# Kernel optimization log

Measured on AMD Instinct MI355X. Metric: run time of the kernel, lower is better.

The kernel has to match this reference:

```python
import jax, jax.numpy as jnp
import numpy as np

B, N, DIM = 8, 4096, 128

def setup_inputs() -> dict:
    key = jax.random.key(0)
    ks = jax.random.split(key, 6)
    s = 1.0 / np.sqrt(DIM)
    return {
        "x": jax.random.normal(ks[0], (B, N, DIM), dtype=jnp.float32),
        "q_global": jax.random.normal(ks[1], (B, N, DIM), dtype=jnp.float32),
        "Wkv": jax.random.normal(ks[2], (DIM, 2 * DIM), dtype=jnp.float32) * s,
        "bkv": jax.random.normal(ks[3], (2 * DIM,), dtype=jnp.float32) * 0.02,
        "Wp": jax.random.normal(ks[4], (DIM, DIM), dtype=jnp.float32) * s,
        "bp": jax.random.normal(ks[5], (DIM,), dtype=jnp.float32) * 0.02,
    }

def reference(x, q_global, Wkv, bkv, Wp, bp):
    # x: [B, n, dim]; kv linear -> split into k, v (each [B, n, dim])
    kv = x @ Wkv + bkv
    k, v = jnp.split(kv, 2, axis=-1)
    dim = x.shape[-1]
    q = q_global * (1.0 / jnp.sqrt(jnp.asarray(dim, x.dtype)))
    # scores = k @ q^T : [B, n, m]; softmax over query axis m (as in source)
    scores = jnp.einsum("bnd,bmd->bnm", k, q)
    attn = jax.nn.softmax(scores, axis=-1)
    # attention @ v : contracts m against v's row index (m == n)
    out = jnp.einsum("bnm,bmd->bnd", attn, v)
    return out @ Wp + bp
```

## Files before the change

kernel.cpp:

```cpp
#include <hip/hip_runtime.h>

typedef __bf16 bf16x8 __attribute__((ext_vector_type(8)));
typedef float f32x4 __attribute__((ext_vector_type(4)));

struct alignas(16) US8 { unsigned short us[8]; };

static __device__ inline unsigned short f2bf(float f) {
  union { float f; unsigned u; } v; v.f = f;
  unsigned r = v.u + 0x7fffu + ((v.u >> 16) & 1u);
  return (unsigned short)(r >> 16);
}

#define NSEQ 4096
#define DIM 128
#define ROWS 32768
#define KH 2

#define EXPC (1.4426950408889634f * 0.08838834764831845f)

__global__ void prep_kernel(const float* __restrict__ Wkv, const float* __restrict__ Wp,
                            unsigned short* __restrict__ wkvT, unsigned short* __restrict__ wpT) {
  const int t = threadIdx.x;
  if (blockIdx.x == 0) {
    for (int d = 0; d < 128; ++d)
      wkvT[t * 128 + d] = f2bf(Wkv[d * 256 + t]);
  } else {
    const int col = t & 127, d0 = (t >> 7) * 64;
    for (int d = d0; d < d0 + 64; ++d)
      wpT[col * 128 + d] = f2bf(Wp[d * 128 + col]);
  }
}

__global__ __launch_bounds__(256, 2) void kv_kernel(
    const float* __restrict__ x, const unsigned short* __restrict__ wkvT,
    const float* __restrict__ bkv, const float* __restrict__ q,
    unsigned short* __restrict__ kout, unsigned short* __restrict__ vtout,
    unsigned short* __restrict__ qo) {
  const int tid = threadIdx.x;
  if (blockIdx.x >= 512) {
    int i = ((blockIdx.x - 512) * 256 + tid) * 8;
    const float4* p = reinterpret_cast<const float4*>(q + i);
    float4 a = p[0], b = p[1];
    US8 o;
    o.us[0]=f2bf(a.x*EXPC); o.us[1]=f2bf(a.y*EXPC); o.us[2]=f2bf(a.z*EXPC); o.us[3]=f2bf(a.w*EXPC);
    o.us[4]=f2bf(b.x*EXPC); o.us[5]=f2bf(b.y*EXPC); o.us[6]=f2bf(b.z*EXPC); o.us[7]=f2bf(b.w*EXPC);
    *reinterpret_cast<US8*>(qo + i) = o;
    return;
  }
  __shared__ __align__(16) unsigned short WT[128 * 136];
  const int wv = tid >> 6, lane = tid & 63, l16 = lane & 15, quad = lane >> 4;
  const int h = blockIdx.x & 1, rb = blockIdx.x >> 1;
  const int row0 = rb * 128;
  const unsigned short* wsrc = wkvT + h * 128 * 128;

  for (int p = 0; p < 8; ++p) {
    int c = p * 256 + tid;
    int col = c >> 4, c16 = c & 15;
    *reinterpret_cast<US8*>(&WT[col * 136 + c16 * 8]) =
        *reinterpret_cast<const US8*>(wsrc + col * 128 + c16 * 8);
  }
  __syncthreads();

  f32x4 acc[2][8];
  for (int rg = 0; rg < 2; ++rg)
    for (int g = 0; g < 8; ++g) acc[rg][g] = f32x4{0.f, 0.f, 0.f, 0.f};
  for (int rg = 0; rg < 2; ++rg) {
    const int arow = row0 + wv * 32 + rg * 16 + l16;
    for (int s = 0; s < 4; ++s) {
      const float4* xp = reinterpret_cast<const float4*>(x + (size_t)arow * DIM + s * 32 + quad * 8);
      float4 u0 = xp[0], u1 = xp[1];
      US8 af;
      af.us[0]=f2bf(u0.x); af.us[1]=f2bf(u0.y); af.us[2]=f2bf(u0.z); af.us[3]=f2bf(u0.w);
      af.us[4]=f2bf(u1.x); af.us[5]=f2bf(u1.y); af.us[6]=f2bf(u1.z); af.us[7]=f2bf(u1.w);
      bf16x8 a = __builtin_bit_cast(bf16x8, af);
      for (int g = 0; g < 8; ++g) {
        bf16x8 bfr = *reinterpret_cast<const bf16x8*>(&WT[(g * 16 + l16) * 136 + s * 32 + quad * 8]);
        acc[rg][g] = __builtin_amdgcn_mfma_f32_16x16x32_bf16(a, bfr, acc[rg][g], 0, 0, 0);
      }
    }
  }

  if (h == 0) {
    for (int rg = 0; rg < 2; ++rg)
      for (int g = 0; g < 8; ++g) {
        float bias = bkv[g * 16 + l16];
        for (int r = 0; r < 4; ++r) {
          int orow = row0 + wv * 32 + rg * 16 + quad * 4 + r;
          kout[(size_t)orow * DIM + g * 16 + l16] = f2bf(acc[rg][g][r] + bias);
        }
      }
  } else {
    __syncthreads();
    unsigned short* LDSt = WT;
    for (int rg = 0; rg < 2; ++rg)
      for (int g = 0; g < 8; ++g) {
        float bias = bkv[128 + g * 16 + l16];
        for (int r = 0; r < 4; ++r)
          LDSt[(g * 16 + l16) * 136 + wv * 32 + rg * 16 + quad * 4 + r] = f2bf(acc[rg][g][r] + bias);
      }
    __syncthreads();
    const int bb = row0 >> 12, n0 = row0 & (NSEQ - 1);
    unsigned short* vb = vtout + (size_t)bb * NSEQ * DIM;
    for (int p = 0; p < 8; ++p) {
      int c = p * 256 + tid;
      int d = c >> 4, c8 = c & 15;
      *reinterpret_cast<US8*>(vb + (size_t)d * NSEQ + n0 + c8 * 8) =
          *reinterpret_cast<const US8*>(&LDSt[d * 136 + c8 * 8]);
    }
  }
}

__global__ __launch_bounds__(256, 2) void attn_kernel(
    const unsigned short* __restrict__ kbuf, const unsigned short* __restrict__ qbuf,
    const unsigned short* __restrict__ vtbuf,
    float* __restrict__ opart, float* __restrict__ lpart) {
  __shared__ __align__(16) unsigned short SH[27136];
  const int tid = threadIdx.x;
  const int wv = tid >> 6, lane = tid & 63, l16 = lane & 15, quad = lane >> 4;
  const int b = blockIdx.x & 7;
  const int t = blockIdx.x >> 3;
  const int q0 = (t & 31) * 128;
  const int kh = t >> 5;
  const int key0 = kh * (NSEQ / KH);
  const unsigned short* kb = kbuf + (size_t)b * NSEQ * DIM;
  const unsigned short* qb = qbuf + (size_t)b * NSEQ * DIM;
  const unsigned short* vtb = vtbuf + (size_t)b * NSEQ * DIM;

  unsigned short* Ksh  = SH;
  unsigned short* VTsh = SH + 8704;
  unsigned short* pp   = SH + 17920 + wv * 2304;

  bf16x8 afrag[2][4];
  for (int rg = 0; rg < 2; ++rg) {
    const int arow = q0 + wv * 32 + rg * 16 + l16;
    for (int s = 0; s < 4; ++s)
      afrag[rg][s] = __builtin_bit_cast(bf16x8,
          *reinterpret_cast<const US8*>(kb + (size_t)arow * DIM + s * 32 + quad * 8));
  }

  f32x4 Oacc[2][8];
  for (int rg = 0; rg < 2; ++rg)
    for (int g = 0; g < 8; ++g) Oacc[rg][g] = f32x4{0.f, 0.f, 0.f, 0.f};
  float lsum[2][4];
  for (int rg = 0; rg < 2; ++rg)
    for (int r = 0; r < 4; ++r) lsum[rg][r] = 0.f;

  for (int it = 0; it < NSEQ / KH / 64; ++it) {
    const int m0 = key0 + it * 64;
    __syncthreads();
    for (int p = 0; p < 4; ++p) {
      int c = p * 256 + tid;
      int row = c >> 4, c16 = c & 15;
      *reinterpret_cast<US8*>(&Ksh[row * 136 + c16 * 8]) =
          *reinterpret_cast<const US8*>(qb + (size_t)(m0 + row) * DIM + c16 * 8);
    }
    for (int p = 0; p < 4; ++p) {
      int c = p * 256 + tid;
      int d = c >> 3, c8 = c & 7;
      *reinterpret_cast<US8*>(&VTsh[d * 72 + c8 * 8]) =
          *reinterpret_cast<const US8*>(vtb + (size_t)d * NSEQ + m0 + c8 * 8);
    }
    __syncthreads();

    f32x4 S[2][4];
    for (int rg = 0; rg < 2; ++rg)
      for (int g = 0; g < 4; ++g) S[rg][g] = f32x4{0.f, 0.f, 0.f, 0.f};
    for (int s = 0; s < 4; ++s)
      for (int g = 0; g < 4; ++g) {
        bf16x8 bfr = *reinterpret_cast<const bf16x8*>(&Ksh[(g * 16 + l16) * 136 + s * 32 + quad * 8]);
        S[0][g] = __builtin_amdgcn_mfma_f32_16x16x32_bf16(afrag[0][s], bfr, S[0][g], 0, 0, 0);
        S[1][g] = __builtin_amdgcn_mfma_f32_16x16x32_bf16(afrag[1][s], bfr, S[1][g], 0, 0, 0);
      }

    for (int rg = 0; rg < 2; ++rg)
      for (int g = 0; g < 4; ++g)
        for (int r = 0; r < 4; ++r) {
          float pv = exp2f(S[rg][g][r]);
          unsigned u = __builtin_bit_cast(unsigned, pv) & 0xffff0000u;
          lsum[rg][r] += __builtin_bit_cast(float, u);
          pp[(rg * 16 + quad * 4 + r) * 72 + g * 16 + l16] = (unsigned short)(u >> 16);
        }

    asm volatile("s_waitcnt lgkmcnt(0)" ::: "memory");

    for (int s2 = 0; s2 < 2; ++s2) {
      bf16x8 pa0 = *reinterpret_cast<const bf16x8*>(&pp[l16 * 72 + s2 * 32 + quad * 8]);
      bf16x8 pa1 = *reinterpret_cast<const bf16x8*>(&pp[(16 + l16) * 72 + s2 * 32 + quad * 8]);
      for (int g = 0; g < 8; ++g) {
        bf16x8 vfr = *reinterpret_cast<const bf16x8*>(&VTsh[(g * 16 + l16) * 72 + s2 * 32 + quad * 8]);
        Oacc[0][g] = __builtin_amdgcn_mfma_f32_16x16x32_bf16(pa0, vfr, Oacc[0][g], 0, 0, 0);
        Oacc[1][g] = __builtin_amdgcn_mfma_f32_16x16x32_bf16(pa1, vfr, Oacc[1][g], 0, 0, 0);
      }
    }
  }

  for (int rg = 0; rg < 2; ++rg)
    for (int r = 0; r < 4; ++r) {
      float v = lsum[rg][r];
      for (int m = 1; m < 16; m <<= 1) v += __shfl_xor(v, m);
      lsum[rg][r] = v;
    }
  if (l16 == 0) {
    float* lp = lpart + (size_t)kh * ROWS + (size_t)b * NSEQ + q0 + wv * 32;
    for (int rg = 0; rg < 2; ++rg)
      for (int r = 0; r < 4; ++r) lp[rg * 16 + quad * 4 + r] = lsum[rg][r];
  }
  float* ob = opart + (size_t)kh * ROWS * DIM + ((size_t)b * NSEQ + q0 + wv * 32) * DIM;
  for (int rg = 0; rg < 2; ++rg)
    for (int g = 0; g < 8; ++g)
      for (int r = 0; r < 4; ++r)
        ob[(rg * 16 + quad * 4 + r) * DIM + g * 16 + l16] = Oacc[rg][g][r];
}

__global__ __launch_bounds__(256, 2) void combine_proj_kernel(
    const float* __restrict__ opart, const float* __restrict__ lpart,
    const unsigned short* __restrict__ wpT, const float* __restrict__ bp,
    float* __restrict__ out) {
  __shared__ __align__(16) unsigned short WT[128 * 136];
  const int tid = threadIdx.x;
  const int wv = tid >> 6, lane = tid & 63, l16 = lane & 15, quad = lane >> 4;
  const int row0 = blockIdx.x * 128;

  for (int p = 0; p < 8; ++p) {
    int c = p * 256 + tid;
    int col = c >> 4, c16 = c & 15;
    *reinterpret_cast<US8*>(&WT[col * 136 + c16 * 8]) =
        *reinterpret_cast<const US8*>(wpT + col * 128 + c16 * 8);
  }
  __syncthreads();

  f32x4 acc[2][8];
  for (int rg = 0; rg < 2; ++rg)
    for (int g = 0; g < 8; ++g) acc[rg][g] = f32x4{0.f, 0.f, 0.f, 0.f};
  for (int rg = 0; rg < 2; ++rg) {
    const int arow = row0 + wv * 32 + rg * 16 + l16;
    float l = lpart[arow] + lpart[ROWS + arow];
    float linv = 1.f / l;
    for (int s = 0; s < 4; ++s) {
      const size_t base = (size_t)arow * DIM + s * 32 + quad * 8;
      float4 s0 = *reinterpret_cast<const float4*>(opart + base);
      float4 s1 = *reinterpret_cast<const float4*>(opart + base + 4);
      for (int buf = 1; buf < KH; ++buf) {
        const float* op = opart + (size_t)buf * ROWS * DIM + base;
        float4 u0 = *reinterpret_cast<const float4*>(op);
        float4 u1 = *reinterpret_cast<const float4*>(op + 4);
        s0.x+=u0.x; s0.y+=u0.y; s0.z+=u0.z; s0.w+=u0.w;
        s1.x+=u1.x; s1.y+=u1.y; s1.z+=u1.z; s1.w+=u1.w;
      }
      US8 af;
      af.us[0]=f2bf(s0.x*linv); af.us[1]=f2bf(s0.y*linv); af.us[2]=f2bf(s0.z*linv); af.us[3]=f2bf(s0.w*linv);
      af.us[4]=f2bf(s1.x*linv); af.us[5]=f2bf(s1.y*linv); af.us[6]=f2bf(s1.z*linv); af.us[7]=f2bf(s1.w*linv);
      bf16x8 a = __builtin_bit_cast(bf16x8, af);
      for (int g = 0; g < 8; ++g) {
        bf16x8 bfr = *reinterpret_cast<const bf16x8*>(&WT[(g * 16 + l16) * 136 + s * 32 + quad * 8]);
        acc[rg][g] = __builtin_amdgcn_mfma_f32_16x16x32_bf16(a, bfr, acc[rg][g], 0, 0, 0);
      }
    }
  }
  for (int rg = 0; rg < 2; ++rg)
    for (int g = 0; g < 8; ++g) {
      float bias = bp[g * 16 + l16];
      for (int r = 0; r < 4; ++r) {
        int orow = row0 + wv * 32 + rg * 16 + quad * 4 + r;
        out[(size_t)orow * DIM + g * 16 + l16] = acc[rg][g][r] + bias;
      }
    }
}

extern "C" void kernel_launch(void* const* d_in, const int* in_sizes, int n_in,
                              void* d_out, int out_size, void* d_ws, size_t ws_size,
                              hipStream_t stream) {
  (void)in_sizes; (void)n_in; (void)out_size; (void)ws_size;
  const float* x   = (const float*)d_in[0];
  const float* qg  = (const float*)d_in[1];
  const float* Wkv = (const float*)d_in[2];
  const float* bkv = (const float*)d_in[3];
  const float* Wp  = (const float*)d_in[4];
  const float* bp  = (const float*)d_in[5];
  float* out = (float*)d_out;

  unsigned short* qbf  = (unsigned short*)d_ws;
  unsigned short* kbf  = qbf + (size_t)ROWS * DIM;
  unsigned short* vtbf = kbf + (size_t)ROWS * DIM;
  unsigned short* wkvT = vtbf + (size_t)ROWS * DIM;
  unsigned short* wpT  = wkvT + 256 * 128;
  float* lpart = (float*)(wpT + 128 * 128);
  float* opart = lpart + (size_t)KH * ROWS;

  hipLaunchKernelGGL(prep_kernel, dim3(2), dim3(256), 0, stream, Wkv, Wp, wkvT, wpT);
  hipLaunchKernelGGL(kv_kernel, dim3(512 + 2048), dim3(256), 0, stream,
                     x, wkvT, bkv, qg, kbf, vtbf, qbf);
  hipLaunchKernelGGL(attn_kernel, dim3(8 * 32 * KH), dim3(256), 0, stream, kbf, qbf, vtbf, opart, lpart);
  hipLaunchKernelGGL(combine_proj_kernel, dim3(ROWS / 128), dim3(256), 0, stream, opart, lpart, wpT, bp, out);
}
```

Measured before the change: 203.7 us.

## Parallelize weight prep, fuse K/V halves, prefetch attention tiles, store partials in bf16

The weight transpose prep now runs across 96 blocks instead of 2 serial blocks. The kv kernel computes K and V for a row block in one block, sharing the x loads and bf16 conversion. The attention loop prefetches the next Q/V tile into registers while computing the current one, and it changes the P scratch layout, likely to reduce LDS bank conflicts. Partial outputs are written as bf16 instead of fp32, which halves that traffic but adds rounding error before the combine step.

```diff
diff --git a/kernel.cpp b/kernel.cpp
--- a/kernel.cpp
+++ b/kernel.cpp
@@ -10,6 +10,9 @@
   unsigned r = v.u + 0x7fffu + ((v.u >> 16) & 1u);
   return (unsigned short)(r >> 16);
 }
+static __device__ inline float bf2f(unsigned short u) {
+  union { unsigned u; float f; } t; t.u = (unsigned)u << 16; return t.f;
+}
 
 #define NSEQ 4096
 #define DIM 128
@@ -21,13 +24,17 @@
 __global__ void prep_kernel(const float* __restrict__ Wkv, const float* __restrict__ Wp,
                             unsigned short* __restrict__ wkvT, unsigned short* __restrict__ wpT) {
   const int t = threadIdx.x;
-  if (blockIdx.x == 0) {
-    for (int d = 0; d < 128; ++d)
-      wkvT[t * 128 + d] = f2bf(Wkv[d * 256 + t]);
+  const int d = (t & 63) * 2;
+  if (blockIdx.x < 64) {
+    const int col = blockIdx.x * 4 + (t >> 6);
+    unsigned short lo = f2bf(Wkv[d * 256 + col]);
+    unsigned short hi = f2bf(Wkv[(d + 1) * 256 + col]);
+    *reinterpret_cast<unsigned*>(&wkvT[col * 128 + d]) = (unsigned)lo | ((unsigned)hi << 16);
   } else {
-    const int col = t & 127, d0 = (t >> 7) * 64;
-    for (int d = d0; d < d0 + 64; ++d)
-      wpT[col * 128 + d] = f2bf(Wp[d * 128 + col]);
+    const int col = (blockIdx.x - 64) * 4 + (t >> 6);
+    unsigned short lo = f2bf(Wp[d * 128 + col]);
+    unsigned short hi = f2bf(Wp[(d + 1) * 128 + col]);
+    *reinterpret_cast<unsigned*>(&wpT[col * 128 + d]) = (unsigned)lo | ((unsigned)hi << 16);
   }
 }
 
@@ -37,8 +44,8 @@
     unsigned short* __restrict__ kout, unsigned short* __restrict__ vtout,
     unsigned short* __restrict__ qo) {
   const int tid = threadIdx.x;
-  if (blockIdx.x >= 512) {
-    int i = ((blockIdx.x - 512) * 256 + tid) * 8;
+  if (blockIdx.x >= 256) {
+    int i = ((blockIdx.x - 256) * 256 + tid) * 8;
     const float4* p = reinterpret_cast<const float4*>(q + i);
     float4 a = p[0], b = p[1];
     US8 o;
@@ -47,23 +54,19 @@
     *reinterpret_cast<US8*>(qo + i) = o;
     return;
   }
-  __shared__ __align__(16) unsigned short WT[128 * 136];
+  __shared__ __align__(16) unsigned short WT[256 * 136];
   const int wv = tid >> 6, lane = tid & 63, l16 = lane & 15, quad = lane >> 4;
-  const int h = blockIdx.x & 1, rb = blockIdx.x >> 1;
-  const int row0 = rb * 128;
-  const unsigned short* wsrc = wkvT + h * 128 * 128;
-
-  for (int p = 0; p < 8; ++p) {
+  const int row0 = blockIdx.x * 128;
+
+  for (int p = 0; p < 16; ++p) {
     int c = p * 256 + tid;
     int col = c >> 4, c16 = c & 15;
     *reinterpret_cast<US8*>(&WT[col * 136 + c16 * 8]) =
-        *reinterpret_cast<const US8*>(wsrc + col * 128 + c16 * 8);
+        *reinterpret_cast<const US8*>(wkvT + col * 128 + c16 * 8);
   }
   __syncthreads();
 
-  f32x4 acc[2][8];
-  for (int rg = 0; rg < 2; ++rg)
-    for (int g = 0; g < 8; ++g) acc[rg][g] = f32x4{0.f, 0.f, 0.f, 0.f};
+  bf16x8 afrag[2][4];
   for (int rg = 0; rg < 2; ++rg) {
     const int arow = row0 + wv * 32 + rg * 16 + l16;
     for (int s = 0; s < 4; ++s) {
@@ -72,48 +75,50 @@
       US8 af;
       af.us[0]=f2bf(u0.x); af.us[1]=f2bf(u0.y); af.us[2]=f2bf(u0.z); af.us[3]=f2bf(u0.w);
       af.us[4]=f2bf(u1.x); af.us[5]=f2bf(u1.y); af.us[6]=f2bf(u1.z); af.us[7]=f2bf(u1.w);
-      bf16x8 a = __builtin_bit_cast(bf16x8, af);
-      for (int g = 0; g < 8; ++g) {
-        bf16x8 bfr = *reinterpret_cast<const bf16x8*>(&WT[(g * 16 + l16) * 136 + s * 32 + quad * 8]);
-        acc[rg][g] = __builtin_amdgcn_mfma_f32_16x16x32_bf16(a, bfr, acc[rg][g], 0, 0, 0);
-      }
-    }
-  }
-
-  if (h == 0) {
-    for (int rg = 0; rg < 2; ++rg)
-      for (int g = 0; g < 8; ++g) {
-        float bias = bkv[g * 16 + l16];
-        for (int r = 0; r < 4; ++r) {
-          int orow = row0 + wv * 32 + rg * 16 + quad * 4 + r;
-          kout[(size_t)orow * DIM + g * 16 + l16] = f2bf(acc[rg][g][r] + bias);
-        }
-      }
-  } else {
-    __syncthreads();
-    unsigned short* LDSt = WT;
-    for (int rg = 0; rg < 2; ++rg)
-      for (int g = 0; g < 8; ++g) {
-        float bias = bkv[128 + g * 16 + l16];
-        for (int r = 0; r < 4; ++r)
-          LDSt[(g * 16 + l16) * 136 + wv * 32 + rg * 16 + quad * 4 + r] = f2bf(acc[rg][g][r] + bias);
-      }
-    __syncthreads();
-    const int bb = row0 >> 12, n0 = row0 & (NSEQ - 1);
-    unsigned short* vb = vtout + (size_t)bb * NSEQ * DIM;
-    for (int p = 0; p < 8; ++p) {
-      int c = p * 256 + tid;
-      int d = c >> 4, c8 = c & 15;
-      *reinterpret_cast<US8*>(vb + (size_t)d * NSEQ + n0 + c8 * 8) =
-          *reinterpret_cast<const US8*>(&LDSt[d * 136 + c8 * 8]);
-    }
+      afrag[rg][s] = __builtin_bit_cast(bf16x8, af);
+    }
+  }
+  f32x4 acc[2][16];
+  for (int rg = 0; rg < 2; ++rg)
+    for (int g = 0; g < 16; ++g) acc[rg][g] = f32x4{0.f, 0.f, 0.f, 0.f};
+  for (int s = 0; s < 4; ++s)
+    for (int g = 0; g < 16; ++g) {
+      bf16x8 bfr = *reinterpret_cast<const bf16x8*>(&WT[(g * 16 + l16) * 136 + s * 32 + quad * 8]);
+      acc[0][g] = __builtin_amdgcn_mfma_f32_16x16x32_bf16(afrag[0][s], bfr, acc[0][g], 0, 0, 0);
+      acc[1][g] = __builtin_amdgcn_mfma_f32_16x16x32_bf16(afrag[1][s], bfr, acc[1][g], 0, 0, 0);
+    }
+
+  for (int rg = 0; rg < 2; ++rg)
+    for (int g = 0; g < 8; ++g) {
+      float bias = bkv[g * 16 + l16];
+      for (int r = 0; r < 4; ++r) {
+        int orow = row0 + wv * 32 + rg * 16 + quad * 4 + r;
+        kout[(size_t)orow * DIM + g * 16 + l16] = f2bf(acc[rg][g][r] + bias);
+      }
+    }
+  __syncthreads();
+  unsigned short* LDSt = WT;
+  for (int rg = 0; rg < 2; ++rg)
+    for (int g = 0; g < 8; ++g) {
+      float bias = bkv[128 + g * 16 + l16];
+      for (int r = 0; r < 4; ++r)
+        LDSt[(g * 16 + l16) * 136 + wv * 32 + rg * 16 + quad * 4 + r] = f2bf(acc[rg][g + 8][r] + bias);
+    }
+  __syncthreads();
+  const int bb = row0 >> 12, n0 = row0 & (NSEQ - 1);
+  unsigned short* vb = vtout + (size_t)bb * NSEQ * DIM;
+  for (int p = 0; p < 8; ++p) {
+    int c = p * 256 + tid;
+    int d = c >> 4, c8 = c & 15;
+    *reinterpret_cast<US8*>(vb + (size_t)d * NSEQ + n0 + c8 * 8) =
+        *reinterpret_cast<const US8*>(&LDSt[d * 136 + c8 * 8]);
   }
 }
 
 __global__ __launch_bounds__(256, 2) void attn_kernel(
     const unsigned short* __restrict__ kbuf, const unsigned short* __restrict__ qbuf,
     const unsigned short* __restrict__ vtbuf,
-    float* __restrict__ opart, float* __restrict__ lpart) {
+    unsigned short* __restrict__ opart, float* __restrict__ lpart) {
   __shared__ __align__(16) unsigned short SH[27136];
   const int tid = threadIdx.x;
   const int wv = tid >> 6, lane = tid & 63, l16 = lane & 15, quad = lane >> 4;
@@ -145,22 +150,34 @@
   for (int rg = 0; rg < 2; ++rg)
     for (int r = 0; r < 4; ++r) lsum[rg][r] = 0.f;
 
-  for (int it = 0; it < NSEQ / KH / 64; ++it) {
-    const int m0 = key0 + it * 64;
+  const int krow = tid >> 4, kc16 = tid & 15;
+  const int vd = tid >> 3, vc8 = tid & 7;
+
+  US8 kreg[4], vreg[4];
+  {
+    const int m0 = key0;
+    for (int p = 0; p < 4; ++p)
+      kreg[p] = *reinterpret_cast<const US8*>(qb + (size_t)(m0 + p * 16 + krow) * DIM + kc16 * 8);
+    for (int p = 0; p < 4; ++p)
+      vreg[p] = *reinterpret_cast<const US8*>(vtb + (size_t)(p * 32 + vd) * NSEQ + m0 + vc8 * 8);
+  }
+
+  const int ITERS = NSEQ / KH / 64;
+  for (int it = 0; it < ITERS; ++it) {
     __syncthreads();
-    for (int p = 0; p < 4; ++p) {
-      int c = p * 256 + tid;
-      int row = c >> 4, c16 = c & 15;
-      *reinterpret_cast<US8*>(&Ksh[row * 136 + c16 * 8]) =
-          *reinterpret_cast<const US8*>(qb + (size_t)(m0 + row) * DIM + c16 * 8);
-    }
-    for (int p = 0; p < 4; ++p) {
-      int c = p * 256 + tid;
-      int d = c >> 3, c8 = c & 7;
-      *reinterpret_cast<US8*>(&VTsh[d * 72 + c8 * 8]) =
-          *reinterpret_cast<const US8*>(vtb + (size_t)d * NSEQ + m0 + c8 * 8);
-    }
+    for (int p = 0; p < 4; ++p)
+      *reinterpret_cast<US8*>(&Ksh[(p * 16 + krow) * 136 + kc16 * 8]) = kreg[p];
+    for (int p = 0; p < 4; ++p)
+      *reinterpret_cast<US8*>(&VTsh[(p * 32 + vd) * 72 + vc8 * 8]) = vreg[p];
     __syncthreads();
+
+    {
+      const int mn = key0 + ((it + 1 < ITERS) ? (it + 1) * 64 : it * 64);
+      for (int p = 0; p < 4; ++p)
+        kreg[p] = *reinterpret_cast<const US8*>(qb + (size_t)(mn + p * 16 + krow) * DIM + kc16 * 8);
+      for (int p = 0; p < 4; ++p)
+        vreg[p] = *reinterpret_cast<const US8*>(vtb + (size_t)(p * 32 + vd) * NSEQ + mn + vc8 * 8);
+    }
 
     f32x4 S[2][4];
     for (int rg = 0; rg < 2; ++rg)
@@ -178,14 +195,14 @@
           float pv = exp2f(S[rg][g][r]);
           unsigned u = __builtin_bit_cast(unsigned, pv) & 0xffff0000u;
           lsum[rg][r] += __builtin_bit_cast(float, u);
-          pp[(rg * 16 + quad * 4 + r) * 72 + g * 16 + l16] = (unsigned short)(u >> 16);
+          pp[(r * 8 + rg * 4 + quad) * 72 + g * 16 + l16] = (unsigned short)(u >> 16);
         }
 
     asm volatile("s_waitcnt lgkmcnt(0)" ::: "memory");
 
     for (int s2 = 0; s2 < 2; ++s2) {
-      bf16x8 pa0 = *reinterpret_cast<const bf16x8*>(&pp[l16 * 72 + s2 * 32 + quad * 8]);
-      bf16x8 pa1 = *reinterpret_cast<const bf16x8*>(&pp[(16 + l16) * 72 + s2 * 32 + quad * 8]);
+      bf16x8 pa0 = *reinterpret_cast<const bf16x8*>(&pp[((l16 & 3) * 8 + (l16 >> 2)) * 72 + s2 * 32 + quad * 8]);
+      bf16x8 pa1 = *reinterpret_cast<const bf16x8*>(&pp[((l16 & 3) * 8 + 4 + (l16 >> 2)) * 72 + s2 * 32 + quad * 8]);
       for (int g = 0; g < 8; ++g) {
         bf16x8 vfr = *reinterpret_cast<const bf16x8*>(&VTsh[(g * 16 + l16) * 72 + s2 * 32 + quad * 8]);
         Oacc[0][g] = __builtin_amdgcn_mfma_f32_16x16x32_bf16(pa0, vfr, Oacc[0][g], 0, 0, 0);
@@ -205,15 +222,15 @@
     for (int rg = 0; rg < 2; ++rg)
       for (int r = 0; r < 4; ++r) lp[rg * 16 + quad * 4 + r] = lsum[rg][r];
   }
-  float* ob = opart + (size_t)kh * ROWS * DIM + ((size_t)b * NSEQ + q0 + wv * 32) * DIM;
+  unsigned short* ob = opart + (size_t)kh * ROWS * DIM + ((size_t)b * NSEQ + q0 + wv * 32) * DIM;
   for (int rg = 0; rg < 2; ++rg)
     for (int g = 0; g < 8; ++g)
       for (int r = 0; r < 4; ++r)
-        ob[(rg * 16 + quad * 4 + r) * DIM + g * 16 + l16] = Oacc[rg][g][r];
+        ob[(rg * 16 + quad * 4 + r) * DIM + g * 16 + l16] = f2bf(Oacc[rg][g][r]);
 }
 
 __global__ __launch_bounds__(256, 2) void combine_proj_kernel(
-    const float* __restrict__ opart, const float* __restrict__ lpart,
+    const unsigned short* __restrict__ opart, const float* __restrict__ lpart,
     const unsigned short* __restrict__ wpT, const float* __restrict__ bp,
     float* __restrict__ out) {
   __shared__ __align__(16) unsigned short WT[128 * 136];
@@ -234,22 +251,14 @@
     for (int g = 0; g < 8; ++g) acc[rg][g] = f32x4{0.f, 0.f, 0.f, 0.f};
   for (int rg = 0; rg < 2; ++rg) {
     const int arow = row0 + wv * 32 + rg * 16 + l16;
-    float l = lpart[arow] + lpart[ROWS + arow];
-    float linv = 1.f / l;
+    float linv = 1.f / (lpart[arow] + lpart[ROWS + arow]);
     for (int s = 0; s < 4; ++s) {
       const size_t base = (size_t)arow * DIM + s * 32 + quad * 8;
-      float4 s0 = *reinterpret_cast<const float4*>(opart + base);
-      float4 s1 = *reinterpret_cast<const float4*>(opart + base + 4);
-      for (int buf = 1; buf < KH; ++buf) {
-        const float* op = opart + (size_t)buf * ROWS * DIM + base;
-        float4 u0 = *reinterpret_cast<const float4*>(op);
-        float4 u1 = *reinterpret_cast<const float4*>(op + 4);
-        s0.x+=u0.x; s0.y+=u0.y; s0.z+=u0.z; s0.w+=u0.w;
-        s1.x+=u1.x; s1.y+=u1.y; s1.z+=u1.z; s1.w+=u1.w;
-      }
+      US8 a0 = *reinterpret_cast<const US8*>(opart + base);
+      US8 a1 = *reinterpret_cast<const US8*>(opart + (size_t)ROWS * DIM + base);
       US8 af;
-      af.us[0]=f2bf(s0.x*linv); af.us[1]=f2bf(s0.y*linv); af.us[2]=f2bf(s0.z*linv); af.us[3]=f2bf(s0.w*linv);
-      af.us[4]=f2bf(s1.x*linv); af.us[5]=f2bf(s1.y*linv); af.us[6]=f2bf(s1.z*linv); af.us[7]=f2bf(s1.w*linv);
+      for (int j = 0; j < 8; ++j)
+        af.us[j] = f2bf((bf2f(a0.us[j]) + bf2f(a1.us[j])) * linv);
       bf16x8 a = __builtin_bit_cast(bf16x8, af);
       for (int g = 0; g < 8; ++g) {
         bf16x8 bfr = *reinterpret_cast<const bf16x8*>(&WT[(g * 16 + l16) * 136 + s * 32 + quad * 8]);
@@ -285,10 +294,10 @@
   unsigned short* wkvT = vtbf + (size_t)ROWS * DIM;
   unsigned short* wpT  = wkvT + 256 * 128;
   float* lpart = (float*)(wpT + 128 * 128);
-  float* opart = lpart + (size_t)KH * ROWS;
-
-  hipLaunchKernelGGL(prep_kernel, dim3(2), dim3(256), 0, stream, Wkv, Wp, wkvT, wpT);
-  hipLaunchKernelGGL(kv_kernel, dim3(512 + 2048), dim3(256), 0, stream,
+  unsigned short* opart = (unsigned short*)(lpart + (size_t)KH * ROWS);
+
+  hipLaunchKernelGGL(prep_kernel, dim3(96), dim3(256), 0, stream, Wkv, Wp, wkvT, wpT);
+  hipLaunchKernelGGL(kv_kernel, dim3(256 + 2048), dim3(256), 0, stream,
                      x, wkvT, bkv, qg, kbf, vtbf, qbf);
   hipLaunchKernelGGL(attn_kernel, dim3(8 * 32 * KH), dim3(256), 0, stream, kbf, qbf, vtbf, opart, lpart);
   hipLaunchKernelGGL(combine_proj_kernel, dim3(ROWS / 128), dim3(256), 0, stream, opart, lpart, wpT, bp, out);
```

Result: slower. 270.5 us (+32.8%).
